# Kernel tuning notes

Measured on AMD Instinct MI355X. Metric: run time of the kernel, lower is better.

Reference implementation:

```python
import jax, jax.numpy as jnp
import numpy as np
import math


def ste_round(x):
    # round with straight-through gradient (identity in bwd)
    return x + jax.lax.stop_gradient(jnp.round(x) - x)


def ste_floor(x):
    return x + jax.lax.stop_gradient(jnp.floor(x) - x)


def _conv(x, w, b):
    # 5x5 stride-2 conv, padding=2 (kernel_size//2), NCHW/OIHW
    y = jax.lax.conv_general_dilated(
        x, w, window_strides=(2, 2), padding=[(2, 2), (2, 2)],
        dimension_numbers=('NCHW', 'OIHW', 'NCHW'))
    return y + b[None, :, None, None]


def _split_conv(x, w, b_int, mul, split=4):
    # 4 redundant sub-convolutions with floor-STE quantized integer weights/biases
    wq = ste_round(w)  # wSTE: round-to-int with STE
    out = 0.0
    for i in range(split):
        out = out + _conv(x, ste_floor((wq + i) / split), ste_floor((b_int + i) / split))
    return out * mul[None, :, None, None]


def _forward(x, w0, b0, w1, b1, w2, b2, w3, b3, mul0, mul1, mul2, mul3,
             relu0, relu1, relu2, md0, md1, md2, md3, ga_left):
    Bits = 8; clp_k = 8; in_scale = 8; scl_k = 3
    relus = [relu0, relu1, relu2]
    clp = [round((2 ** Bits - 1) / r * 2 ** (16 + clp_k)) for r in relus]
    scl = [math.floor((r + 2 ** (scl_k - 1)) / 2 ** scl_k) for r in relus]

    # quantize input to uint8 range
    x = jnp.clip(ste_round(x * 2 ** in_scale), 0, 255)

    # ---- layer 0 ----
    x = _split_conv(x, w0, ste_round(b0 * 2 ** in_scale), mul0)
    x = ste_floor((x + 2.0 ** (md0 - 1 + in_scale - clp_k)) / 2.0 ** (md0 + in_scale - clp_k))
    x = jnp.clip(x, 0, clp[0])
    x = ste_floor((ste_round(x * scl[0]) + 2.0 ** (15 + clp_k - scl_k)) / 2.0 ** (16 + clp_k - scl_k))

    # ---- layers 1, 2 ----
    for w_, b_, mul_, md_, idx in ((w1, b1, mul1, md1, 1), (w2, b2, mul2, md2, 2)):
        x = _split_conv(x, w_, ste_round(b_), mul_)
        x = ste_floor((x + 2.0 ** (md_ - 1 - clp_k)) / 2.0 ** (md_ - clp_k))
        x = jnp.clip(x, 0, clp[idx])
        x = ste_floor((ste_round(x * scl[idx]) + 2.0 ** (15 + clp_k - scl_k)) / 2.0 ** (16 + clp_k - scl_k))

    # ---- layer 3 (latent) ----
    x = _split_conv(x, w3, ste_round(b3), mul3)
    x = ste_floor((x + 2.0 ** (md3 - 1 - ga_left)) / 2.0 ** (md3 - ga_left))
    return x


def setup_inputs():
    key = jax.random.key(0)
    ks = jax.random.split(key, 16)
    N, M = 192, 320
    d = {}
    d['x'] = jax.random.uniform(ks[0], (4, 3, 512, 512), dtype=jnp.float32)
    # float weights whose round() gives small ints (integerized LIC weights)
    d['w0'] = jax.random.normal(ks[1], (N, 3, 5, 5), dtype=jnp.float32) * 3.0
    d['b0'] = jax.random.normal(ks[2], (N,), dtype=jnp.float32)
    d['w1'] = jax.random.normal(ks[3], (N, N, 5, 5), dtype=jnp.float32) * 3.0
    d['b1'] = jax.random.normal(ks[4], (N,), dtype=jnp.float32) * 16.0
    d['w2'] = jax.random.normal(ks[5], (N, N, 5, 5), dtype=jnp.float32) * 3.0
    d['b2'] = jax.random.normal(ks[6], (N,), dtype=jnp.float32) * 16.0
    d['w3'] = jax.random.normal(ks[7], (M, N, 5, 5), dtype=jnp.float32) * 3.0
    d['b3'] = jax.random.normal(ks[8], (M,), dtype=jnp.float32) * 16.0
    # per-channel integer-valued fixed-point multipliers
    d['mul0'] = jax.random.randint(ks[9], (N,), 1, 64).astype(jnp.float32)
    d['mul1'] = jax.random.randint(ks[10], (N,), 1, 64).astype(jnp.float32)
    d['mul2'] = jax.random.randint(ks[11], (N,), 1, 64).astype(jnp.float32)
    d['mul3'] = jax.random.randint(ks[12], (M,), 1, 64).astype(jnp.float32)
    d['relu0'] = 65536; d['relu1'] = 65536; d['relu2'] = 65536
    d['md0'] = 7; d['md1'] = 15; d['md2'] = 15; d['md3'] = 10
    d['ga_left'] = 4
    return d


def reference(x, w0, b0, w1, b1, w2, b2, w3, b3, mul0, mul1, mul2, mul3,
              relu0, relu1, relu2, md0, md1, md2, md3, ga_left):
    return _forward(x, w0, b0, w1, b1, w2, b2, w3, b3, mul0, mul1, mul2, mul3,
                    relu0, relu1, relu2, md0, md1, md2, md3, ga_left)
```

## Files before the change

### kernel.cpp

```cpp
#include <hip/hip_runtime.h>
#include <hip/hip_bf16.h>

typedef int i32x4 __attribute__((ext_vector_type(4)));
typedef unsigned int u32;
typedef unsigned long long u64;
typedef long long ll;

__device__ __forceinline__ void load_lds16(const void* g, void* l) {
  __builtin_amdgcn_global_load_lds(
      (const __attribute__((address_space(1))) u32*)g,
      (__attribute__((address_space(3))) u32*)l, 16, 0, 0);
}

__global__ __launch_bounds__(256) void prep_all(
    const float* __restrict__ w0, const float* __restrict__ w1,
    const float* __restrict__ w2, const float* __restrict__ w3,
    signed char* __restrict__ w0q, signed char* __restrict__ w1p,
    signed char* __restrict__ w2p, signed char* __restrict__ w3p,
    signed char* __restrict__ zbuf,
    int* __restrict__ totw0, int* __restrict__ totw1,
    int* __restrict__ totw2, int* __restrict__ totw3)
{
  __shared__ signed char ldsw[8 * 4800];
  const int blk = blockIdx.x;
  const int tid = threadIdx.x;

  if (blk < 88) {
    const float* wsrc; signed char* wdst; int* tot; int MF, sub;
    if (blk < 24)      { wsrc = w1; wdst = w1p; tot = totw1; MF = 12; sub = blk; }
    else if (blk < 48) { wsrc = w2; wdst = w2p; tot = totw2; MF = 12; sub = blk - 24; }
    else               { wsrc = w3; wdst = w3p; tot = totw3; MF = 20; sub = blk - 48; }
    const int mf = sub >> 1, half = sub & 1, colbase = half * 8;
    const int ocb = mf * 16 + colbase;
    for (int o = 0; o < 8; o++) {
      const float* src = wsrc + (size_t)(ocb + o) * 4800;
      int s = 0;
      for (int j = tid; j < 4800; j += 256) {
        int v = (int)rintf(src[j]);
        ldsw[o * 4800 + j] = (signed char)v;
        s += v;
      }
      atomicAdd(&tot[ocb + o], s);
    }
    __syncthreads();
    for (int u = tid; u < 9600; u += 256) {
      int eu = u & 3, colL = (u >> 2) & 7, q = (u >> 5) & 3, t = u >> 7;
      int tap = t / 3, ch = t - 3 * tap;
      int ci0 = ch * 64 + q * 16 + eu * 4;
      const signed char* sp = ldsw + colL * 4800 + tap;
      u32 wv = 0;
      #pragma unroll
      for (int bb = 0; bb < 4; bb++)
        wv |= ((u32)(unsigned char)sp[(ci0 + bb) * 25]) << (8 * bb);
      *(u32*)(wdst + ((size_t)t * MF + mf) * 1024 +
              (q * 16 + colbase + colL) * 16 + eu * 4) = wv;
    }
  } else {
    if (tid < 128) ((u64*)zbuf)[tid] = 0x8080808080808080ULL;
    for (int i = tid; i < 24576; i += 256) {
      int e = i & 15, colA = (i >> 4) & 15, q = (i >> 8) & 3, t = i >> 10;
      int mf = t % 12, ch = t / 12;
      signed char v = 0;
      if (e < 15 && (ch == 0 || q == 0)) {
        int ky = (ch == 0) ? q : 4;
        int ci = e / 5, kx = e - ci * 5;
        v = (signed char)(int)rintf(
            w0[((mf * 16 + colA) * 3 + ci) * 25 + ky * 5 + kx]);
      }
      w0q[i] = v;
    }
    for (int oc = tid; oc < 192; oc += 256) {
      const float* p = w0 + (size_t)oc * 75;
      int s = 0;
      #pragma unroll 5
      for (int j = 0; j < 75; j++) s += (int)rintf(p[j]);
      totw0[oc] = s;
    }
  }
}

__global__ __launch_bounds__(192, 3) void conv0F(
    const float* __restrict__ x, const signed char* __restrict__ wq,
    const float* __restrict__ bias, const float* __restrict__ mulv,
    const int* __restrict__ totw,
    const int* __restrict__ reluP, const int* __restrict__ mdP,
    unsigned char* __restrict__ outA)
{
  __shared__ signed char ilds[3][5][132];

  const int tid = threadIdx.x;
  const int lane = tid & 63;
  const int col = lane & 15;
  const int quad = lane >> 4;
  const int w = tid >> 6;
  const int blk = blockIdx.x;
  const int oxblk = blk & 3;
  const int oy = (blk >> 2) & 255;
  const int b = blk >> 10;
  const int oxbase = oxblk * 64;

  i32x4 afr[2][4];
  #pragma unroll
  for (int ch = 0; ch < 2; ch++)
    #pragma unroll
    for (int i = 0; i < 4; i++)
      afr[ch][i] = *(const i32x4*)(wq + ch * 12288 + (w * 4 + i) * 1024 + lane * 16);

  const float* xb = x + (size_t)b * 3 * 512 * 512;
  for (int i = tid; i < 990; i += 192) {
    int j = i % 66; int t = i / 66; int r = t % 5; int ci = t / 5;
    int iy = 2 * oy - 2 + r;
    int ix = 2 * oxbase - 2 + 2 * j;
    int v0 = -128, v1 = -128;
    if ((unsigned)iy < 512u) {
      const float* row = xb + ((size_t)ci * 512 + iy) * 512;
      if ((unsigned)ix < 512u) {
        float xv = rintf(row[ix] * 256.0f);
        v0 = (int)fminf(fmaxf(xv, 0.0f), 255.0f) - 128;
      }
      if ((unsigned)(ix + 1) < 512u) {
        float xv = rintf(row[ix + 1] * 256.0f);
        v1 = (int)fminf(fmaxf(xv, 0.0f), 255.0f) - 128;
      }
    }
    *(unsigned short*)&ilds[ci][r][2 * j] =
        (unsigned short)((v0 & 0xFF) | ((v1 & 0xFF) << 8));
  }
  __syncthreads();

  i32x4 acc[4][4];
  #pragma unroll
  for (int fm = 0; fm < 4; fm++)
    #pragma unroll
    for (int fn = 0; fn < 4; fn++) acc[fm][fn] = (i32x4){0, 0, 0, 0};

  #pragma unroll
  for (int ch = 0; ch < 2; ch++) {
    const int row = (ch == 0) ? quad : 4;
    i32x4 bfr[4];
    #pragma unroll
    for (int fn = 0; fn < 4; fn++) {
      const int xb2 = 2 * (fn * 16 + col);
      const int o8 = (xb2 & 3) * 8;
      const int ab = xb2 & ~3;
      u64 w0_, w1_, w2_;
      {
        const u32* p0 = (const u32*)&ilds[0][row][ab];
        const u32* p1 = (const u32*)&ilds[1][row][ab];
        const u32* p2 = (const u32*)&ilds[2][row][ab];
        w0_ = (u64)p0[0] | ((u64)p0[1] << 32);
        w1_ = (u64)p1[0] | ((u64)p1[1] << 32);
        w2_ = (u64)p2[0] | ((u64)p2[1] << 32);
      }
      u32 a0 = (u32)(w0_ >> o8);
      u32 a1 = ((u32)(w0_ >> (o8 + 32)) & 0xFFu) | (((u32)(w1_ >> o8)) << 8);
      u32 a2 = ((u32)(w1_ >> (o8 + 24)) & 0xFFFFu) | (((u32)(w2_ >> o8)) << 16);
      u32 a3 = (u32)(w2_ >> (o8 + 16));
      bfr[fn] = (i32x4){(int)a0, (int)a1, (int)a2, (int)a3};
    }
    #pragma unroll
    for (int fm = 0; fm < 4; fm++)
      #pragma unroll
      for (int fn = 0; fn < 4; fn++)
        acc[fm][fn] = __builtin_amdgcn_mfma_i32_16x16x64_i8(
            afr[ch][fm], bfr[fn], acc[fm][fn], 0, 0, 0);
  }

  const size_t pix0 = ((size_t)(b * 256 + oy)) * 256 + oxbase;
  const int rl = reluP[0];
  const int sh = mdP[0];
  const ll clpv_ll = llrint(255.0 / (double)rl * 16777216.0);
  const int clpv = clpv_ll > 0x7FFFFFFFLL ? 0x7FFFFFFF : (int)clpv_ll;
  const int sclv = (int)((rl + 4) >> 3);
  const int rnd = 1 << (sh - 1);
  #pragma unroll
  for (int fm = 0; fm < 4; fm++) {
    const int oc0 = w * 64 + fm * 16 + quad * 4;
    int bim[4], mu32[4];
    #pragma unroll
    for (int r = 0; r < 4; r++) {
      int bi = (int)llrintf(bias[oc0 + r] * 256.0f) + 128 * totw[oc0 + r];
      mu32[r] = (int)llrintf(mulv[oc0 + r]);
      bim[r] = bi * mu32[r];
    }
    #pragma unroll
    for (int fn = 0; fn < 4; fn++) {
      const size_t pix = pix0 + fn * 16 + col;
      u32 wd = 0;
      #pragma unroll
      for (int r = 0; r < 4; r++) {
        int vi = acc[fm][fn][r] * mu32[r] + bim[r];
        int y = (vi + rnd) >> sh;
        y = y < 0 ? 0 : (y > clpv ? clpv : y);
        y = (y * sclv + (1 << 20)) >> 21;
        wd |= (((u32)y ^ 0x80u) & 0xFFu) << (8 * r);
      }
      *(u32*)(outA + pix * 192 + oc0) = wd;
    }
  }
}

template <int COUT, int HIN, int WIN, int HOUT, int WOUT, int MW,
          int KSPLIT, bool DIRECT>
__global__ __launch_bounds__(MW * 64, 3) void convS(
    const signed char* __restrict__ act, const signed char* __restrict__ wp,
    const float* __restrict__ bias, const float* __restrict__ mulv,
    const int* __restrict__ totw,
    const int* __restrict__ reluP, const int* __restrict__ mdP,
    const signed char* __restrict__ zbuf,
    unsigned char* __restrict__ outA, int* __restrict__ outP)
{
  constexpr int CIN = 192;
  constexpr int PASSES = 4;
  constexpr int MAXP = (PASSES + MW - 1) / MW;
  constexpr int SAe = MW * 4096;
  constexpr int TX = WOUT / 16;
  constexpr int TYB = HOUT / 4;
  constexpr int TPP = 25 / KSPLIT;
  constexpr int NSTEP = TPP * 3;
  constexpr int PSZ = 4 * HOUT * WOUT * COUT;
  static_assert(MW * 64 == COUT, "M covers COUT");

  __shared__ __align__(16) char smem[2 * 4096];

  const int tid = threadIdx.x;
  const int lane = tid & 63;
  const int col = lane & 15;
  const int quad = lane >> 4;
  const int w = tid >> 6;
  const int part = blockIdx.y;

  int bx = blockIdx.x;
  const int tx = bx % TX; bx /= TX;
  const int ty = bx % TYB;
  const int b = bx / TYB;
  const int ox0 = tx * 16;
  const int oy0 = ty * 4;

  const signed char* bptr[MAXP];
  int bmx[MAXP], bmy[MAXP];
  #pragma unroll
  for (int k = 0; k < MAXP; k++) {
    int p = w + k * MW;
    if (p >= PASSES) break;
    int oxv = ox0 + col;
    int oyv = oy0 + p;
    bptr[k] = act + ((size_t)b * HIN * WIN + (size_t)(2 * oyv) * WIN + 2 * oxv) * CIN
              + quad * 16;
    int mx = 0, my = 0;
    #pragma unroll
    for (int kk = 0; kk < 5; kk++) {
      if ((unsigned)(2 * oxv + kk - 2) < (unsigned)WIN) mx |= 1 << kk;
      if ((unsigned)(2 * oyv + kk - 2) < (unsigned)HIN) my |= 1 << kk;
    }
    bmx[k] = mx; bmy[k] = my;
  }

  int kxS, kyS, chS;

  auto stage = [&](int sel) {
    const int offB = ((kyS - 2) * WIN + (kxS - 2)) * CIN + chS * 64;
    #pragma unroll
    for (int k = 0; k < MAXP; k++) {
      int p = w + k * MW;
      if (p >= PASSES) break;
      bool v = ((bmx[k] >> kxS) & 1) && ((bmy[k] >> kyS) & 1);
      const signed char* g = v ? (bptr[k] + offB) : (zbuf + quad * 16);
      load_lds16(g, smem + sel * 4096 + p * 1024);
    }
  };
  auto adv = [&]() {
    chS++;
    if (chS == 3) { chS = 0; kxS++; if (kxS == 5) { kxS = 0; kyS++; } }
  };

  i32x4 acc[4][4];
  #pragma unroll
  for (int fm = 0; fm < 4; fm++)
    #pragma unroll
    for (int fn = 0; fn < 4; fn++) acc[fm][fn] = (i32x4){0, 0, 0, 0};

  const int tap0 = part * TPP;
  kyS = tap0 / 5; kxS = tap0 - 5 * kyS; chS = 0;
  stage(0);
  adv();
  const signed char* aptr = wp + (size_t)(tap0 * 3) * SAe + w * 4096 + lane * 16;
  i32x4 aA[4], aB[4];
  #pragma unroll
  for (int i = 0; i < 4; i++) aA[i] = *(const i32x4*)(aptr + i * 1024);

  auto comp = [&](int base, i32x4 (&a)[4]) {
    const char* pB = smem + base + lane * 16;
    i32x4 bfr[4];
    #pragma unroll
    for (int i = 0; i < 4; i++)
      bfr[i] = *(const i32x4*)(pB + i * 1024);
    #pragma unroll
    for (int fm = 0; fm < 4; fm++)
      #pragma unroll
      for (int fn = 0; fn < 4; fn++)
        acc[fm][fn] = __builtin_amdgcn_mfma_i32_16x16x64_i8(
            a[fm], bfr[fn], acc[fm][fn], 0, 0, 0);
  };

  int sl = 0;
  #pragma unroll 1
  for (; sl + 1 < NSTEP; sl += 2) {
    __syncthreads();
    stage(1); adv();
    aptr += SAe;
    #pragma unroll
    for (int i = 0; i < 4; i++) aB[i] = *(const i32x4*)(aptr + i * 1024);
    comp(0, aA);

    __syncthreads();
    if (sl + 2 < NSTEP) {
      stage(0); adv();
      aptr += SAe;
      #pragma unroll
      for (int i = 0; i < 4; i++) aA[i] = *(const i32x4*)(aptr + i * 1024);
    }
    comp(4096, aB);
  }
  if (sl < NSTEP) {
    __syncthreads();
    comp(0, aA);
  }

  if constexpr (DIRECT) {
    const int rl = reluP[0];
    const int sh = mdP[0] - 8;
    const ll clpv = llrint(255.0 / (double)rl * 16777216.0);
    const ll sclv = (ll)((rl + 4) >> 3);
    #pragma unroll
    for (int fm = 0; fm < 4; fm++) {
      const int oc0 = w * 64 + fm * 16 + quad * 4;
      ll bi[4], mu[4];
      #pragma unroll
      for (int r = 0; r < 4; r++) {
        bi[r] = llrintf(bias[oc0 + r]) + 128LL * totw[oc0 + r];
        mu[r] = llrintf(mulv[oc0 + r]);
      }
      #pragma unroll
      for (int fn = 0; fn < 4; fn++) {
        const int oyv = oy0 + fn;
        const int oxv = ox0 + col;
        u32 wd = 0;
        #pragma unroll
        for (int r = 0; r < 4; r++) {
          ll vi = ((ll)acc[fm][fn][r] + bi[r]) * mu[r];
          ll y = (vi + (1LL << (sh - 1))) >> sh;
          y = y < 0 ? 0LL : (y > clpv ? clpv : y);
          y = (y * sclv + (1LL << 20)) >> 21;
          wd |= (((u32)y ^ 0x80u) & 0xFFu) << (8 * r);
        }
        *(u32*)(outA + ((size_t)((b * HOUT + oyv) * WOUT + oxv)) * COUT + oc0) = wd;
      }
    }
  } else {
    int* pout = outP + (size_t)part * PSZ;
    #pragma unroll
    for (int fm = 0; fm < 4; fm++) {
      const int oc0 = w * 64 + fm * 16 + quad * 4;
      #pragma unroll
      for (int fn = 0; fn < 4; fn++) {
        const int oyv = oy0 + fn;
        const int oxv = ox0 + col;
        *(i32x4*)(pout + ((size_t)((b * HOUT + oyv) * WOUT + oxv)) * COUT + oc0) =
            acc[fm][fn];
      }
    }
  }
}

__global__ __launch_bounds__(256) void reduce2(
    const int* __restrict__ partP, const float* __restrict__ bias,
    const float* __restrict__ mulv, const int* __restrict__ totw,
    const int* __restrict__ reluP, const int* __restrict__ mdP,
    unsigned char* __restrict__ outA)
{
  const int gid = blockIdx.x * 256 + threadIdx.x;
  const int PSZ4 = 4 * 64 * 64 * 192 / 4;
  const int4* pp = (const int4*)partP;
  int4 sv = pp[gid];
  #pragma unroll
  for (int p = 1; p < 5; p++) {
    int4 v = pp[(size_t)p * PSZ4 + gid];
    sv.x += v.x; sv.y += v.y; sv.z += v.z; sv.w += v.w;
  }
  int sa[4] = {sv.x, sv.y, sv.z, sv.w};
  const int oc0 = (gid * 4) % 192;
  const int rl = reluP[0];
  const int sh = mdP[0] - 8;
  const ll clpv = llrint(255.0 / (double)rl * 16777216.0);
  const ll sclv = (ll)((rl + 4) >> 3);
  u32 wd = 0;
  #pragma unroll
  for (int r = 0; r < 4; r++) {
    ll bi = llrintf(bias[oc0 + r]) + 128LL * totw[oc0 + r];
    ll mu = llrintf(mulv[oc0 + r]);
    ll vi = ((ll)sa[r] + bi) * mu;
    ll y = (vi + (1LL << (sh - 1))) >> sh;
    y = y < 0 ? 0LL : (y > clpv ? clpv : y);
    y = (y * sclv + (1LL << 20)) >> 21;
    wd |= (((u32)y ^ 0x80u) & 0xFFu) << (8 * r);
  }
  ((u32*)outA)[gid] = wd;
}

__global__ __launch_bounds__(256) void reduce3(
    const int* __restrict__ partP, const float* __restrict__ b3,
    const float* __restrict__ mul3, const int* __restrict__ totw3,
    const int* __restrict__ mdP, const int* __restrict__ gaP,
    float* __restrict__ outF)
{
  const int gid = blockIdx.x * 256 + threadIdx.x;
  int t = gid;
  const int ox = t & 31; t >>= 5;
  const int oy = t & 31; t >>= 5;
  const int oc = t % 320;
  const int b  = t / 320;
  const int PSZ = 4 * 32 * 32 * 320;
  const size_t src = ((size_t)((b * 32 + oy) * 32 + ox)) * 320 + oc;
  ll s = 0;
  #pragma unroll
  for (int p = 0; p < 5; p++) s += partP[(size_t)p * PSZ + src];
  const int sh = mdP[0] - gaP[0];
  const ll bi = llrintf(b3[oc]) + 128LL * totw3[oc];
  const ll mu = llrintf(mul3[oc]);
  const ll y = ((s + bi) * mu + (1LL << (sh - 1))) >> sh;
  outF[gid] = (float)y;
}

extern "C" void kernel_launch(void* const* d_in, const int* in_sizes, int n_in,
                              void* d_out, int out_size, void* d_ws, size_t ws_size,
                              hipStream_t stream)
{
  const float* x    = (const float*)d_in[0];
  const float* w0   = (const float*)d_in[1];
  const float* b0   = (const float*)d_in[2];
  const float* w1   = (const float*)d_in[3];
  const float* b1   = (const float*)d_in[4];
  const float* w2   = (const float*)d_in[5];
  const float* b2   = (const float*)d_in[6];
  const float* w3   = (const float*)d_in[7];
  const float* b3   = (const float*)d_in[8];
  const float* mul0 = (const float*)d_in[9];
  const float* mul1 = (const float*)d_in[10];
  const float* mul2 = (const float*)d_in[11];
  const float* mul3 = (const float*)d_in[12];
  const int* relu0  = (const int*)d_in[13];
  const int* relu1  = (const int*)d_in[14];
  const int* relu2  = (const int*)d_in[15];
  const int* md0    = (const int*)d_in[16];
  const int* md1    = (const int*)d_in[17];
  const int* md2    = (const int*)d_in[18];
  const int* md3    = (const int*)d_in[19];
  const int* ga     = (const int*)d_in[20];

  char* ws = (char*)d_ws;
  size_t off = 0;
  signed char* zbuf = (signed char*)(ws + off); off += 1024;
  signed char* w0q  = (signed char*)(ws + off); off += 24576;
  signed char* w1p  = (signed char*)(ws + off); off += 921600;
  signed char* w2p  = (signed char*)(ws + off); off += 921600;
  signed char* w3p  = (signed char*)(ws + off); off += 1536000;
  int*         totw1= (int*)        (ws + off); off += 192 * 4;
  int*         totw2= (int*)        (ws + off); off += 192 * 4;
  int*         totw3= (int*)        (ws + off); off += 320 * 4;
  int*         totw0= (int*)        (ws + off); off += 192 * 4;
  unsigned char* act1 = (unsigned char*)(ws + off); off += (size_t)4 * 256 * 256 * 192;
  unsigned char* act2 = (unsigned char*)(ws + off); off += (size_t)4 * 128 * 128 * 192;
  unsigned char* act3 = (unsigned char*)(ws + off); off += (size_t)4 * 64 * 64 * 192;
  int*         partl  = (int*)(ws + off); off += (size_t)5 * 4 * 64 * 64 * 192 * 4;
  (void)ws_size; (void)in_sizes; (void)n_in; (void)out_size;

  hipMemsetAsync(totw1, 0, (192 + 192 + 320 + 192) * 4, stream);
  prep_all<<<89, 256, 0, stream>>>(w0, w1, w2, w3, w0q, w1p, w2p, w3p,
                                   zbuf, totw0, totw1, totw2, totw3);
  conv0F<<<4096, 192, 0, stream>>>(x, w0q, b0, mul0, totw0, relu0, md0, act1);
  convS<192, 256, 256, 128, 128, 3, 1, true><<<dim3(1024, 1), 192, 0, stream>>>(
      (const signed char*)act1, w1p, b1, mul1, totw1, relu1, md1, zbuf, act2, nullptr);
  convS<192, 128, 128, 64, 64, 3, 5, false><<<dim3(256, 5), 192, 0, stream>>>(
      (const signed char*)act2, w2p, b2, mul2, totw2, relu2, md2, zbuf, nullptr, partl);
  reduce2<<<3072, 256, 0, stream>>>(partl, b2, mul2, totw2, relu2, md2, act3);
  convS<320, 64, 64, 32, 32, 5, 5, false><<<dim3(64, 5), 320, 0, stream>>>(
      (const signed char*)act3, w3p, b3, mul3, totw3, nullptr, md3, zbuf, nullptr, partl);
  reduce3<<<5120, 256, 0, stream>>>(partl, b3, mul3, totw3, md3, ga, (float*)d_out);
}
```

Baseline: 341.4 us.

## Stage a whole kernel tap per pipeline step to cut barriers

The conv loop's LDS double-buffer now holds all three 64-channel chunks of a tap per stage, instead of staging one chunk at a time. That means one __syncthreads per tap rather than one per chunk, and each stage issues more global-to-LDS loads spread across the waves. Per-pass pointers and y-masks are collapsed into a single base pointer plus packed bitmasks, which cuts register use. In exchange LDS grows from 8 KB to 24 KB per block, which may limit occupancy. The weight prefetch also reads one chunk past the tap range on the final iteration.

```diff
diff --git a/kernel.cpp b/kernel.cpp
--- a/kernel.cpp
+++ b/kernel.cpp
@@ -212,16 +212,18 @@
 {
   constexpr int CIN = 192;
   constexpr int PASSES = 4;
-  constexpr int MAXP = (PASSES + MW - 1) / MW;
   constexpr int SAe = MW * 4096;
   constexpr int TX = WOUT / 16;
   constexpr int TYB = HOUT / 4;
   constexpr int TPP = 25 / KSPLIT;
-  constexpr int NSTEP = TPP * 3;
+  constexpr int NLOAD = PASSES * 3;
+  constexpr int MAXL = (NLOAD + MW - 1) / MW;
+  constexpr int BUF = NLOAD * 1024;
+  constexpr int ROWSTEP = 2 * WIN * CIN;
   constexpr int PSZ = 4 * HOUT * WOUT * COUT;
   static_assert(MW * 64 == COUT, "M covers COUT");
 
-  __shared__ __align__(16) char smem[2 * 4096];
+  __shared__ __align__(16) char smem[2 * BUF];
 
   const int tid = threadIdx.x;
   const int lane = tid & 63;
@@ -237,42 +239,39 @@
   const int ox0 = tx * 16;
   const int oy0 = ty * 4;
 
-  const signed char* bptr[MAXP];
-  int bmx[MAXP], bmy[MAXP];
-  #pragma unroll
-  for (int k = 0; k < MAXP; k++) {
-    int p = w + k * MW;
-    if (p >= PASSES) break;
-    int oxv = ox0 + col;
-    int oyv = oy0 + p;
-    bptr[k] = act + ((size_t)b * HIN * WIN + (size_t)(2 * oyv) * WIN + 2 * oxv) * CIN
-              + quad * 16;
-    int mx = 0, my = 0;
-    #pragma unroll
-    for (int kk = 0; kk < 5; kk++) {
-      if ((unsigned)(2 * oxv + kk - 2) < (unsigned)WIN) mx |= 1 << kk;
-      if ((unsigned)(2 * oyv + kk - 2) < (unsigned)HIN) my |= 1 << kk;
-    }
-    bmx[k] = mx; bmy[k] = my;
-  }
-
-  int kxS, kyS, chS;
+  const signed char* base0 =
+      act + ((size_t)b * HIN * WIN + (size_t)(2 * oy0) * WIN + 2 * (ox0 + col)) * CIN
+      + quad * 16;
+  int bmx = 0;
+  #pragma unroll
+  for (int kk = 0; kk < 5; kk++)
+    if ((unsigned)(2 * (ox0 + col) + kk - 2) < (unsigned)WIN) bmx |= 1 << kk;
+  int bmyPack = 0;
+  #pragma unroll
+  for (int p = 0; p < PASSES; p++) {
+    #pragma unroll
+    for (int kk = 0; kk < 5; kk++)
+      if ((unsigned)(2 * (oy0 + p) + kk - 2) < (unsigned)HIN)
+        bmyPack |= 1 << (p * 5 + kk);
+  }
+
+  const int tap0 = part * TPP;
+  int kyS = tap0 / 5, kxS = tap0 - 5 * kyS;
 
   auto stage = [&](int sel) {
-    const int offB = ((kyS - 2) * WIN + (kxS - 2)) * CIN + chS * 64;
-    #pragma unroll
-    for (int k = 0; k < MAXP; k++) {
-      int p = w + k * MW;
-      if (p >= PASSES) break;
-      bool v = ((bmx[k] >> kxS) & 1) && ((bmy[k] >> kyS) & 1);
-      const signed char* g = v ? (bptr[k] + offB) : (zbuf + quad * 16);
-      load_lds16(g, smem + sel * 4096 + p * 1024);
-    }
+    const int offB = ((kyS - 2) * WIN + (kxS - 2)) * CIN;
+    #pragma unroll
+    for (int k = 0; k < MAXL; k++) {
+      int j = w + k * MW;
+      if (j >= NLOAD) break;
+      int p = j / 3, c = j - 3 * p;
+      bool v = ((bmx >> kxS) & 1) && ((bmyPack >> (p * 5 + kyS)) & 1);
+      const signed char* g =
+          v ? (base0 + (size_t)p * ROWSTEP + offB + c * 64) : (zbuf + quad * 16);
+      load_lds16(g, smem + sel * BUF + j * 1024);
+    }
+    kxS++; if (kxS == 5) { kxS = 0; kyS++; }
   };
-  auto adv = [&]() {
-    chS++;
-    if (chS == 3) { chS = 0; kxS++; if (kxS == 5) { kxS = 0; kyS++; } }
-  };
 
   i32x4 acc[4][4];
   #pragma unroll
@@ -280,21 +279,11 @@
     #pragma unroll
     for (int fn = 0; fn < 4; fn++) acc[fm][fn] = (i32x4){0, 0, 0, 0};
 
-  const int tap0 = part * TPP;
-  kyS = tap0 / 5; kxS = tap0 - 5 * kyS; chS = 0;
-  stage(0);
-  adv();
-  const signed char* aptr = wp + (size_t)(tap0 * 3) * SAe + w * 4096 + lane * 16;
-  i32x4 aA[4], aB[4];
-  #pragma unroll
-  for (int i = 0; i < 4; i++) aA[i] = *(const i32x4*)(aptr + i * 1024);
-
-  auto comp = [&](int base, i32x4 (&a)[4]) {
-    const char* pB = smem + base + lane * 16;
+  auto comp = [&](const char* pB, i32x4 (&a)[4]) {
     i32x4 bfr[4];
     #pragma unroll
     for (int i = 0; i < 4; i++)
-      bfr[i] = *(const i32x4*)(pB + i * 1024);
+      bfr[i] = *(const i32x4*)(pB + i * 3072);
     #pragma unroll
     for (int fm = 0; fm < 4; fm++)
       #pragma unroll
@@ -303,28 +292,27 @@
             a[fm], bfr[fn], acc[fm][fn], 0, 0, 0);
   };
 
-  int sl = 0;
+  stage(0);
+  const signed char* aptr = wp + (size_t)(tap0 * 3) * SAe + w * 4096 + lane * 16;
+  i32x4 aC[4], aN[4];
+  #pragma unroll
+  for (int i = 0; i < 4; i++) aC[i] = *(const i32x4*)(aptr + i * 1024);
+
   #pragma unroll 1
-  for (; sl + 1 < NSTEP; sl += 2) {
+  for (int t = 0; t < TPP; t++) {
+    const int sel = t & 1;
     __syncthreads();
-    stage(1); adv();
-    aptr += SAe;
-    #pragma unroll
-    for (int i = 0; i < 4; i++) aB[i] = *(const i32x4*)(aptr + i * 1024);
-    comp(0, aA);
-
-    __syncthreads();
-    if (sl + 2 < NSTEP) {
-      stage(0); adv();
+    if (t + 1 < TPP) stage(sel ^ 1);
+    const char* base = smem + sel * BUF + lane * 16;
+    #pragma unroll
+    for (int c = 0; c < 3; c++) {
       aptr += SAe;
       #pragma unroll
-      for (int i = 0; i < 4; i++) aA[i] = *(const i32x4*)(aptr + i * 1024);
-    }
-    comp(4096, aB);
-  }
-  if (sl < NSTEP) {
-    __syncthreads();
-    comp(0, aA);
+      for (int i = 0; i < 4; i++) aN[i] = *(const i32x4*)(aptr + i * 1024);
+      comp(base + c * 1024, aC);
+      #pragma unroll
+      for (int i = 0; i < 4; i++) aC[i] = aN[i];
+    }
   }
 
   if constexpr (DIRECT) {
```

Result: slower. 366.1 us (+7.3%).

## Add dedicated producer wave with 4-deep LDS ring for convS activations

Applied to the files above, without the earlier changes.

Adds one extra wavefront per block that only issues global-to-LDS loads for the activation tiles. It uses a 4-slot LDS ring buffer and is coordinated by raw s_barrier and vmcnt waits. The MFMA waves no longer stage loads themselves, so load latency can overlap compute across three stages instead of double buffering. In exchange, LDS per block grows, each block has an extra wave, and the hand-counted barrier matching between producer and consumers is fragile.

```diff
diff --git a/kernel.cpp b/kernel.cpp
--- a/kernel.cpp
+++ b/kernel.cpp
@@ -202,7 +202,7 @@
 
 template <int COUT, int HIN, int WIN, int HOUT, int WOUT, int MW,
           int KSPLIT, bool DIRECT>
-__global__ __launch_bounds__(MW * 64, 3) void convS(
+__global__ __launch_bounds__((MW + 1) * 64, 3) void convS(
     const signed char* __restrict__ act, const signed char* __restrict__ wp,
     const float* __restrict__ bias, const float* __restrict__ mulv,
     const int* __restrict__ totw,
@@ -212,7 +212,6 @@
 {
   constexpr int CIN = 192;
   constexpr int PASSES = 4;
-  constexpr int MAXP = (PASSES + MW - 1) / MW;
   constexpr int SAe = MW * 4096;
   constexpr int TX = WOUT / 16;
   constexpr int TYB = HOUT / 4;
@@ -220,8 +219,9 @@
   constexpr int NSTEP = TPP * 3;
   constexpr int PSZ = 4 * HOUT * WOUT * COUT;
   static_assert(MW * 64 == COUT, "M covers COUT");
-
-  __shared__ __align__(16) char smem[2 * 4096];
+  static_assert(NSTEP >= 4, "pipeline depth");
+
+  __shared__ __align__(16) char smem[4 * 4096];
 
   const int tid = threadIdx.x;
   const int lane = tid & 63;
@@ -236,43 +236,53 @@
   const int b = bx / TYB;
   const int ox0 = tx * 16;
   const int oy0 = ty * 4;
-
-  const signed char* bptr[MAXP];
-  int bmx[MAXP], bmy[MAXP];
-  #pragma unroll
-  for (int k = 0; k < MAXP; k++) {
-    int p = w + k * MW;
-    if (p >= PASSES) break;
-    int oxv = ox0 + col;
-    int oyv = oy0 + p;
-    bptr[k] = act + ((size_t)b * HIN * WIN + (size_t)(2 * oyv) * WIN + 2 * oxv) * CIN
-              + quad * 16;
-    int mx = 0, my = 0;
-    #pragma unroll
-    for (int kk = 0; kk < 5; kk++) {
-      if ((unsigned)(2 * oxv + kk - 2) < (unsigned)WIN) mx |= 1 << kk;
-      if ((unsigned)(2 * oyv + kk - 2) < (unsigned)HIN) my |= 1 << kk;
-    }
-    bmx[k] = mx; bmy[k] = my;
-  }
-
-  int kxS, kyS, chS;
-
-  auto stage = [&](int sel) {
-    const int offB = ((kyS - 2) * WIN + (kxS - 2)) * CIN + chS * 64;
-    #pragma unroll
-    for (int k = 0; k < MAXP; k++) {
-      int p = w + k * MW;
-      if (p >= PASSES) break;
-      bool v = ((bmx[k] >> kxS) & 1) && ((bmy[k] >> kyS) & 1);
-      const signed char* g = v ? (bptr[k] + offB) : (zbuf + quad * 16);
-      load_lds16(g, smem + sel * 4096 + p * 1024);
-    }
-  };
-  auto adv = [&]() {
-    chS++;
-    if (chS == 3) { chS = 0; kxS++; if (kxS == 5) { kxS = 0; kyS++; } }
-  };
+  const int tap0 = part * TPP;
+
+  if (w == MW) {
+    const signed char* bptr[PASSES];
+    int bmy[PASSES];
+    int bmx = 0;
+    const int oxv = ox0 + col;
+    #pragma unroll
+    for (int kk = 0; kk < 5; kk++)
+      if ((unsigned)(2 * oxv + kk - 2) < (unsigned)WIN) bmx |= 1 << kk;
+    #pragma unroll
+    for (int p = 0; p < PASSES; p++) {
+      const int oyv = oy0 + p;
+      bptr[p] = act + ((size_t)b * HIN * WIN + (size_t)(2 * oyv) * WIN + 2 * oxv) * CIN
+                + quad * 16;
+      int my = 0;
+      #pragma unroll
+      for (int kk = 0; kk < 5; kk++)
+        if ((unsigned)(2 * oyv + kk - 2) < (unsigned)HIN) my |= 1 << kk;
+      bmy[p] = my;
+    }
+    int kyS = tap0 / 5, kxS = tap0 - 5 * kyS, chS = 0;
+    auto stage = [&](int sel) {
+      const int offB = ((kyS - 2) * WIN + (kxS - 2)) * CIN + chS * 64;
+      #pragma unroll
+      for (int p = 0; p < PASSES; p++) {
+        bool v = ((bmx >> kxS) & 1) && ((bmy[p] >> kyS) & 1);
+        const signed char* g = v ? (bptr[p] + offB) : (zbuf + quad * 16);
+        load_lds16(g, smem + sel * 4096 + p * 1024);
+      }
+      chS++;
+      if (chS == 3) { chS = 0; kxS++; if (kxS == 5) { kxS = 0; kyS++; } }
+    };
+    stage(0); stage(1); stage(2);
+    asm volatile("s_waitcnt vmcnt(8)" ::: "memory");
+    asm volatile("s_barrier" ::: "memory");
+    #pragma unroll 1
+    for (int sl = 0; sl + 1 < NSTEP; ++sl) {
+      if (sl + 3 < NSTEP) stage((sl + 3) & 3);
+      const int rem = NSTEP - 2 - sl;
+      if (rem >= 2)      asm volatile("s_waitcnt vmcnt(8)" ::: "memory");
+      else if (rem == 1) asm volatile("s_waitcnt vmcnt(4)" ::: "memory");
+      else               asm volatile("s_waitcnt vmcnt(0)" ::: "memory");
+      asm volatile("s_barrier" ::: "memory");
+    }
+    return;
+  }
 
   i32x4 acc[4][4];
   #pragma unroll
@@ -280,10 +290,6 @@
     #pragma unroll
     for (int fn = 0; fn < 4; fn++) acc[fm][fn] = (i32x4){0, 0, 0, 0};
 
-  const int tap0 = part * TPP;
-  kyS = tap0 / 5; kxS = tap0 - 5 * kyS; chS = 0;
-  stage(0);
-  adv();
   const signed char* aptr = wp + (size_t)(tap0 * 3) * SAe + w * 4096 + lane * 16;
   i32x4 aA[4], aB[4];
   #pragma unroll
@@ -303,28 +309,25 @@
             a[fm], bfr[fn], acc[fm][fn], 0, 0, 0);
   };
 
+  asm volatile("s_barrier" ::: "memory");
   int sl = 0;
   #pragma unroll 1
   for (; sl + 1 < NSTEP; sl += 2) {
-    __syncthreads();
-    stage(1); adv();
     aptr += SAe;
     #pragma unroll
     for (int i = 0; i < 4; i++) aB[i] = *(const i32x4*)(aptr + i * 1024);
-    comp(0, aA);
-
-    __syncthreads();
+    comp((sl & 3) * 4096, aA);
+    asm volatile("s_barrier" ::: "memory");
     if (sl + 2 < NSTEP) {
-      stage(0); adv();
       aptr += SAe;
       #pragma unroll
       for (int i = 0; i < 4; i++) aA[i] = *(const i32x4*)(aptr + i * 1024);
     }
-    comp(4096, aB);
+    comp(((sl + 1) & 3) * 4096, aB);
+    if (sl + 2 < NSTEP) asm volatile("s_barrier" ::: "memory");
   }
   if (sl < NSTEP) {
-    __syncthreads();
-    comp(0, aA);
+    comp((sl & 3) * 4096, aA);
   }
 
   if constexpr (DIRECT) {
@@ -479,12 +482,12 @@
   prep_all<<<89, 256, 0, stream>>>(w0, w1, w2, w3, w0q, w1p, w2p, w3p,
                                    zbuf, totw0, totw1, totw2, totw3);
   conv0F<<<4096, 192, 0, stream>>>(x, w0q, b0, mul0, totw0, relu0, md0, act1);
-  convS<192, 256, 256, 128, 128, 3, 1, true><<<dim3(1024, 1), 192, 0, stream>>>(
+  convS<192, 256, 256, 128, 128, 3, 1, true><<<dim3(1024, 1), 256, 0, stream>>>(
       (const signed char*)act1, w1p, b1, mul1, totw1, relu1, md1, zbuf, act2, nullptr);
-  convS<192, 128, 128, 64, 64, 3, 5, false><<<dim3(256, 5), 192, 0, stream>>>(
+  convS<192, 128, 128, 64, 64, 3, 5, false><<<dim3(256, 5), 256, 0, stream>>>(
       (const signed char*)act2, w2p, b2, mul2, totw2, relu2, md2, zbuf, nullptr, partl);
   reduce2<<<3072, 256, 0, stream>>>(partl, b2, mul2, totw2, relu2, md2, act3);
-  convS<320, 64, 64, 32, 32, 5, 5, false><<<dim3(64, 5), 320, 0, stream>>>(
+  convS<320, 64, 64, 32, 32, 5, 5, false><<<dim3(64, 5), 384, 0, stream>>>(
       (const signed char*)act3, w3p, b3, mul3, totw3, nullptr, md3, zbuf, nullptr, partl);
   reduce3<<<5120, 256, 0, stream>>>(partl, b3, mul3, totw3, md3, ga, (float*)d_out);
 }
```

After: 342.9 us. Within noise of the previous version (+0.4%).
